# Kernel tuning notes

Hardware: AMD Instinct MI355X
Metric: run time of the kernel (lower is better)

The kernel has to match this reference:

```python
import jax, jax.numpy as jnp
import numpy as np

N, DIM = 4096, 1024

def setup_inputs() -> dict:
    key = jax.random.key(0)
    ks = jax.random.split(key, 5)
    scale = 1.0 / np.sqrt(DIM)
    return {
        "x": jax.random.normal(ks[0], (N, DIM), dtype=jnp.float32),
        "Wq": jax.random.normal(ks[1], (DIM, DIM), dtype=jnp.float32) * scale,
        "bq": jax.random.normal(ks[2], (DIM,), dtype=jnp.float32) * 0.01,
        "Wk": jax.random.normal(ks[3], (DIM, DIM), dtype=jnp.float32) * scale,
        "bk": jax.random.normal(ks[4], (DIM,), dtype=jnp.float32) * 0.01,
    }

def reference(x, Wq, bq, Wk, bk):
    # torch nn.Linear: y = x @ W.T + b
    q = x @ Wq.T + bq            # [N, D]
    k = x @ Wk.T + bk            # [N, D]
    scores = q @ k.T             # [N, N] (no 1/sqrt(d) scaling, as in source)
    attn = jax.nn.softmax(scores, axis=-1)
    return attn @ x              # weighted pooling over raw x (no value proj)
```

## Files before the change

kernel.cpp:

```cpp
#include <hip/hip_runtime.h>
#include <hip/hip_bf16.h>
#include <hip/hip_fp16.h>
#include <stdint.h>


using half8   = __attribute__((ext_vector_type(8))) _Float16;
using float4v = __attribute__((ext_vector_type(4))) float;
using int4v   = __attribute__((ext_vector_type(4))) int;

#define QS        (6.0f / 32768.0f)
#define INV_S     (32768.0f / 6.0f)
#define INV_S256  (128.0f / 6.0f)
#define C_HH      (65536.0f * QS * QS)
#define C_X       (256.0f * QS * QS)

#define SX        (6.0f / 32768.0f)
#define SW        (0.25f / 32768.0f)
#define P_HH      (65536.0f * SX * SW)
#define P_X       (256.0f * SX * SW)

#define GLOAD_LDS16(gptr, ldsptr)                                              \
  __builtin_amdgcn_global_load_lds(                                            \
      (__attribute__((address_space(1))) void*)(uintptr_t)(gptr),              \
      (__attribute__((address_space(3))) void*)(unsigned)(uintptr_t)(ldsptr),  \
      16, 0, 0)

__global__ __launch_bounds__(256, 2) void gemm_s_stats(
    const int8_t* __restrict__ Ahi, const int8_t* __restrict__ Alo,
    const int8_t* __restrict__ Bhi, const int8_t* __restrict__ Blo,
    _Float16* __restrict__ E, float2* __restrict__ stats)
{
  __shared__ __align__(16) int8_t sAh[128 * 64];
  __shared__ __align__(16) int8_t sAl[128 * 64];
  __shared__ __align__(16) int8_t sBh[128 * 64];
  __shared__ __align__(16) int8_t sBl[128 * 64];

  const int tid  = threadIdx.x;
  const int wave = tid >> 6;
  const int lane = tid & 63;
  const int quad = lane >> 4;
  const int t16  = lane & 15;
  const int wm   = wave & 1;
  const int wn   = wave >> 1;
  const int row0 = blockIdx.y * 128;
  const int col0 = blockIdx.x * 128;

  const int seg  = lane & 3;
  const int rsub = lane >> 2;

  int4v hh[4][4], cc[4][4];
#pragma unroll
  for (int i = 0; i < 4; ++i)
#pragma unroll
    for (int j = 0; j < 4; ++j) {
      hh[i][j] = (int4v){0, 0, 0, 0};
      cc[i][j] = (int4v){0, 0, 0, 0};
    }

  for (int k0 = 0; k0 < 1024; k0 += 64) {
#pragma unroll
    for (int r = 0; r < 2; ++r) {
      const int trow = r * 64 + wave * 16;
      const size_t goffA = (size_t)(row0 + trow + rsub) * 2048 + k0 + seg * 16;
      const size_t goffB = (size_t)(col0 + trow + rsub) * 2048 + k0 + seg * 16;
      GLOAD_LDS16(Ahi + goffA, &sAh[trow * 64]);
      GLOAD_LDS16(Alo + goffA, &sAl[trow * 64]);
      GLOAD_LDS16(Bhi + goffB, &sBh[trow * 64]);
      GLOAD_LDS16(Blo + goffB, &sBl[trow * 64]);
    }
    __syncthreads();

    int4v ah[4], al[4], bh[4], bl[4];
#pragma unroll
    for (int i = 0; i < 4; ++i) {
      const int ar = (wm * 64 + i * 16 + t16) * 64 + quad * 16;
      ah[i] = *(const int4v*)&sAh[ar];
      al[i] = *(const int4v*)&sAl[ar];
    }
#pragma unroll
    for (int j = 0; j < 4; ++j) {
      const int br = (wn * 64 + j * 16 + t16) * 64 + quad * 16;
      bh[j] = *(const int4v*)&sBh[br];
      bl[j] = *(const int4v*)&sBl[br];
    }

#pragma unroll
    for (int i = 0; i < 4; ++i)
#pragma unroll
      for (int j = 0; j < 4; ++j) {
        hh[i][j] = __builtin_amdgcn_mfma_i32_16x16x64_i8(ah[i], bh[j], hh[i][j], 0, 0, 0);
        cc[i][j] = __builtin_amdgcn_mfma_i32_16x16x64_i8(ah[i], bl[j], cc[i][j], 0, 0, 0);
        cc[i][j] = __builtin_amdgcn_mfma_i32_16x16x64_i8(al[i], bh[j], cc[i][j], 0, 0, 0);
      }
    __syncthreads();
  }

  float* red = (float*)sAh;

  float vv[4][4][4];
  float rmax[4][4];
#pragma unroll
  for (int i = 0; i < 4; ++i)
#pragma unroll
    for (int r = 0; r < 4; ++r) {
      float mx = -3.0e38f;
#pragma unroll
      for (int j = 0; j < 4; ++j) {
        float v = C_HH * (float)hh[i][j][r] + C_X * (float)cc[i][j][r];
        vv[i][j][r] = v;
        mx = fmaxf(mx, v);
      }
      mx = fmaxf(mx, __shfl_xor(mx, 1));
      mx = fmaxf(mx, __shfl_xor(mx, 2));
      mx = fmaxf(mx, __shfl_xor(mx, 4));
      mx = fmaxf(mx, __shfl_xor(mx, 8));
      rmax[i][r] = mx;
    }
  if (t16 == 0) {
#pragma unroll
    for (int i = 0; i < 4; ++i)
#pragma unroll
      for (int r = 0; r < 4; ++r)
        red[wn * 128 + wm * 64 + i * 16 + quad * 4 + r] = rmax[i][r];
  }
  __syncthreads();

  float mrow[4][4];
#pragma unroll
  for (int i = 0; i < 4; ++i)
#pragma unroll
    for (int r = 0; r < 4; ++r) {
      const int row = wm * 64 + i * 16 + quad * 4 + r;
      mrow[i][r] = fmaxf(red[row], red[128 + row]);
    }

  float rsum[4][4];
#pragma unroll
  for (int i = 0; i < 4; ++i)
#pragma unroll
    for (int r = 0; r < 4; ++r) {
      float s = 0.f;
#pragma unroll
      for (int j = 0; j < 4; ++j) {
        float e = __expf(vv[i][j][r] - mrow[i][r]);
        vv[i][j][r] = e;
        s += e;
      }
      s += __shfl_xor(s, 1);
      s += __shfl_xor(s, 2);
      s += __shfl_xor(s, 4);
      s += __shfl_xor(s, 8);
      rsum[i][r] = s;
    }
  if (t16 == 0) {
#pragma unroll
    for (int i = 0; i < 4; ++i)
#pragma unroll
      for (int r = 0; r < 4; ++r)
        red[256 + wn * 128 + wm * 64 + i * 16 + quad * 4 + r] = rsum[i][r];
  }
  __syncthreads();

#pragma unroll
  for (int i = 0; i < 4; ++i) {
#pragma unroll
    for (int j = 0; j < 4; ++j) {
#pragma unroll
      for (int r = 0; r < 4; ++r) {
        const int crow = row0 + wm * 64 + i * 16 + quad * 4 + r;
        const int ccol = col0 + wn * 64 + j * 16 + t16;
        E[(size_t)crow * 4096 + ccol] = (_Float16)vv[i][j][r];
      }
    }
  }
  if (wn == 0 && t16 == 0) {
#pragma unroll
    for (int i = 0; i < 4; ++i)
#pragma unroll
      for (int r = 0; r < 4; ++r) {
        const int row = wm * 64 + i * 16 + quad * 4 + r;
        const float l = red[256 + row] + red[256 + 128 + row];
        stats[(size_t)(row0 + row) * 32 + blockIdx.x] =
            make_float2(mrow[i][r], l);
      }
  }
}

__global__ __launch_bounds__(256, 2) void gemm_proj_i8(
    const int8_t* __restrict__ Ahi, const int8_t* __restrict__ Alo,
    const int8_t* __restrict__ Bhi, const int8_t* __restrict__ Blo,
    const float* __restrict__ biasQ, const float* __restrict__ biasK,
    int8_t* __restrict__ Ch, int8_t* __restrict__ Cl)
{
  __shared__ __align__(16) int8_t sAh[128 * 64];
  __shared__ __align__(16) int8_t sAl[128 * 64];
  __shared__ __align__(16) int8_t sBh[128 * 64];
  __shared__ __align__(16) int8_t sBl[128 * 64];

  const int tid  = threadIdx.x;
  const int wave = tid >> 6;
  const int lane = tid & 63;
  const int quad = lane >> 4;
  const int t16  = lane & 15;
  const int wm   = wave & 1;
  const int wn   = wave >> 1;
  const int row0 = blockIdx.y * 128;
  const int col0 = blockIdx.x * 128;

  const int seg  = lane & 3;
  const int rsub = lane >> 2;

  int4v hh[4][4], cc[4][4];
#pragma unroll
  for (int i = 0; i < 4; ++i)
#pragma unroll
    for (int j = 0; j < 4; ++j) {
      hh[i][j] = (int4v){0, 0, 0, 0};
      cc[i][j] = (int4v){0, 0, 0, 0};
    }

  for (int k0 = 0; k0 < 1024; k0 += 64) {
#pragma unroll
    for (int r = 0; r < 2; ++r) {
      const int trow = r * 64 + wave * 16;
      const size_t goffA = (size_t)(row0 + trow + rsub) * 1024 + k0 + seg * 16;
      const size_t goffB = (size_t)(col0 + trow + rsub) * 1024 + k0 + seg * 16;
      GLOAD_LDS16(Ahi + goffA, &sAh[trow * 64]);
      GLOAD_LDS16(Alo + goffA, &sAl[trow * 64]);
      GLOAD_LDS16(Bhi + goffB, &sBh[trow * 64]);
      GLOAD_LDS16(Blo + goffB, &sBl[trow * 64]);
    }
    __syncthreads();

    int4v ah[4], al[4], bh[4], bl[4];
#pragma unroll
    for (int i = 0; i < 4; ++i) {
      const int ar = (wm * 64 + i * 16 + t16) * 64 + quad * 16;
      ah[i] = *(const int4v*)&sAh[ar];
      al[i] = *(const int4v*)&sAl[ar];
    }
#pragma unroll
    for (int j = 0; j < 4; ++j) {
      const int br = (wn * 64 + j * 16 + t16) * 64 + quad * 16;
      bh[j] = *(const int4v*)&sBh[br];
      bl[j] = *(const int4v*)&sBl[br];
    }

#pragma unroll
    for (int i = 0; i < 4; ++i)
#pragma unroll
      for (int j = 0; j < 4; ++j) {
        hh[i][j] = __builtin_amdgcn_mfma_i32_16x16x64_i8(ah[i], bh[j], hh[i][j], 0, 0, 0);
        cc[i][j] = __builtin_amdgcn_mfma_i32_16x16x64_i8(ah[i], bl[j], cc[i][j], 0, 0, 0);
        cc[i][j] = __builtin_amdgcn_mfma_i32_16x16x64_i8(al[i], bh[j], cc[i][j], 0, 0, 0);
      }
    __syncthreads();
  }

#pragma unroll
  for (int i = 0; i < 4; ++i) {
#pragma unroll
    for (int j = 0; j < 4; ++j) {
      const int ccol = col0 + wn * 64 + j * 16 + t16;
      const float* bp = (ccol < 1024) ? biasQ : (biasK - 1024);
#pragma unroll
      for (int r = 0; r < 4; ++r) {
        const int crow = row0 + wm * 64 + i * 16 + quad * 4 + r;
        float v = P_HH * (float)hh[i][j][r] + P_X * (float)cc[i][j][r] + bp[ccol];
        int hi = (int)lrintf(v * INV_S256);
        hi = hi > 127 ? 127 : (hi < -127 ? -127 : hi);
        int lo = (int)lrintf(v * INV_S - 256.0f * (float)hi);
        lo = lo > 127 ? 127 : (lo < -127 ? -127 : lo);
        Ch[(size_t)crow * 2048 + ccol] = (int8_t)hi;
        Cl[(size_t)crow * 2048 + ccol] = (int8_t)lo;
      }
    }
  }
}

__global__ __launch_bounds__(512) void gemm_av(
    const uint16_t* __restrict__ E, const uint16_t* __restrict__ B,
    const float2* __restrict__ stats, float* __restrict__ out)
{
  __shared__ __align__(16) uint16_t stage[16384];
  __shared__ float betaS[128 * 33];

  const int L      = blockIdx.x;
  const int xcd    = L & 7;
  const int rest   = L >> 3;
  const int colb   = rest & 7;
  const int bandHi = rest >> 3;
  const int band   = xcd + 8 * bandHi;
  const int row0   = band * 128;
  const int col0   = colb * 128;

  const int tid  = threadIdx.x;
  const int wave = tid >> 6;
  const int z    = wave >> 2;
  const int gw   = wave & 3;
  const int lane = tid & 63;
  const int quad = lane >> 4;
  const int t16  = lane & 15;
  const int wm   = gw & 1;
  const int wn   = gw >> 1;
  const int seg  = lane & 3;
  const int rsub = lane >> 2;

  if (tid < 128) {
    const int row = row0 + tid;
    float2 st[32];
    float m = -3.0e38f;
#pragma unroll
    for (int t = 0; t < 32; ++t) {
      st[t] = stats[(size_t)row * 32 + t];
      m = fmaxf(m, st[t].x);
    }
    float l = 0.f;
#pragma unroll
    for (int t = 0; t < 32; ++t) l += st[t].y * __expf(st[t].x - m);
    const float inv = 1.0f / l;
#pragma unroll
    for (int t = 0; t < 32; ++t)
      betaS[tid * 33 + t] = __expf(st[t].x - m) * inv;
  }
  __syncthreads();

  uint16_t* sA = &stage[z * 8192];
  uint16_t* sB = &stage[z * 8192 + 4096];

  float4v acc[4][4];
#pragma unroll
  for (int i = 0; i < 4; ++i)
#pragma unroll
    for (int j = 0; j < 4; ++j)
      acc[i][j] = (float4v){0.f, 0.f, 0.f, 0.f};

  for (int tt = 0; tt < 16; ++tt) {
    const int t = z * 16 + tt;
    _Float16 bb[4];
#pragma unroll
    for (int i = 0; i < 4; ++i)
      bb[i] = (_Float16)betaS[(wm * 64 + i * 16 + t16) * 33 + t];

#pragma unroll
    for (int kk = 0; kk < 4; ++kk) {
      const int k0 = t * 128 + kk * 32;
#pragma unroll
      for (int r = 0; r < 2; ++r) {
        const int trow = r * 64 + gw * 16;
        const size_t goffA = (size_t)(row0 + trow + rsub) * 4096 + k0 + seg * 8;
        const size_t goffB = (size_t)(col0 + trow + rsub) * 4096 + k0 + seg * 8;
        GLOAD_LDS16(E + goffA, &sA[trow * 32]);
        GLOAD_LDS16(B + goffB, &sB[trow * 32]);
      }
      __syncthreads();

      half8 af[4], bf[4];
#pragma unroll
      for (int i = 0; i < 4; ++i) {
        af[i] = *(const half8*)&sA[(wm * 64 + i * 16 + t16) * 32 + quad * 8];
        half8 bs;
#pragma unroll
        for (int c = 0; c < 8; ++c) bs[c] = bb[i];
        af[i] = af[i] * bs;
      }
#pragma unroll
      for (int j = 0; j < 4; ++j)
        bf[j] = *(const half8*)&sB[(wn * 64 + j * 16 + t16) * 32 + quad * 8];

#pragma unroll
      for (int i = 0; i < 4; ++i)
#pragma unroll
        for (int j = 0; j < 4; ++j)
          acc[i][j] = __builtin_amdgcn_mfma_f32_16x16x32_f16(af[i], bf[j], acc[i][j], 0, 0, 0);
      __syncthreads();
    }
  }

  float* xfer = (float*)stage;
#pragma unroll
  for (int h = 0; h < 2; ++h) {
    if (z == 1) {
#pragma unroll
      for (int i = 2 * h; i < 2 * h + 2; ++i)
#pragma unroll
        for (int j = 0; j < 4; ++j)
#pragma unroll
          for (int r = 0; r < 4; ++r) {
            const int e = (i - 2 * h) * 16 + j * 4 + r;
            xfer[e * 256 + gw * 64 + lane] = acc[i][j][r];
          }
    }
    __syncthreads();
    if (z == 0) {
#pragma unroll
      for (int i = 2 * h; i < 2 * h + 2; ++i)
#pragma unroll
        for (int j = 0; j < 4; ++j)
#pragma unroll
          for (int r = 0; r < 4; ++r) {
            const int e = (i - 2 * h) * 16 + j * 4 + r;
            acc[i][j][r] += xfer[e * 256 + gw * 64 + lane];
          }
    }
    __syncthreads();
  }

  if (z == 0) {
#pragma unroll
    for (int i = 0; i < 4; ++i) {
#pragma unroll
      for (int j = 0; j < 4; ++j) {
        const int ccol = col0 + wn * 64 + j * 16 + t16;
#pragma unroll
        for (int r = 0; r < 4; ++r) {
          const int crow = row0 + wm * 64 + i * 16 + quad * 4 + r;
          out[(size_t)crow * 1024 + ccol] = acc[i][j][r];
        }
      }
    }
  }
}

__global__ __launch_bounds__(256) void quantT(
    const float* __restrict__ x, const float* __restrict__ Wq,
    const float* __restrict__ Wk,
    int8_t* __restrict__ xhi, int8_t* __restrict__ xlo,
    int8_t* __restrict__ whi, int8_t* __restrict__ wlo,
    uint16_t* __restrict__ xT)
{
  if (blockIdx.x < 6144) {
    int i = blockIdx.x * 256 + threadIdx.x;
    const float* src; int8_t* dh; int8_t* dl; int idx; float s256, s;
    if (i < 1048576)      { src = x;  idx = i;           dh = xhi; dl = xlo;
                            s256 = INV_S256; s = INV_S; }
    else if (i < 1310720) { src = Wq; idx = i - 1048576; dh = whi; dl = wlo;
                            s256 = 512.0f; s = 131072.0f; }
    else                  { src = Wk; idx = i - 1310720; dh = whi + 1048576;
                            dl = wlo + 1048576; s256 = 512.0f; s = 131072.0f; }
    float4 v = ((const float4*)src)[idx];
    float vv[4] = {v.x, v.y, v.z, v.w};
    int hp = 0, lp = 0;
#pragma unroll
    for (int c = 0; c < 4; ++c) {
      int h = (int)lrintf(vv[c] * s256);
      h = h > 127 ? 127 : (h < -127 ? -127 : h);
      int l = (int)lrintf(vv[c] * s - 256.0f * (float)h);
      l = l > 127 ? 127 : (l < -127 ? -127 : l);
      hp |= (h & 0xff) << (8 * c);
      lp |= (l & 0xff) << (8 * c);
    }
    ((int*)dh)[idx] = hp;
    ((int*)dl)[idx] = lp;
  } else {
    __shared__ float tile[32][33];
    const int tb = blockIdx.x - 6144;
    const int bx = tb & 31;
    const int by = tb >> 5;
    const int tx = threadIdx.x & 31;
    const int ty = threadIdx.x >> 5;
#pragma unroll
    for (int p = 0; p < 4; ++p) {
      const int row = by * 32 + ty + p * 8;
      tile[ty + p * 8][tx] = x[(size_t)row * 1024 + bx * 32 + tx];
    }
    __syncthreads();
#pragma unroll
    for (int p = 0; p < 4; ++p) {
      const int oc = ty + p * 8;
      __half hv = __float2half_rn(tile[tx][oc]);
      xT[(size_t)(bx * 32 + oc) * 4096 + by * 32 + tx] = *(uint16_t*)&hv;
    }
  }
}

extern "C" void kernel_launch(void* const* d_in, const int* in_sizes, int n_in,
                              void* d_out, int out_size, void* d_ws, size_t ws_size,
                              hipStream_t stream) {
  const int N = 4096, D = 1024;
  const float* x  = (const float*)d_in[0];
  const float* Wq = (const float*)d_in[1];
  const float* bq = (const float*)d_in[2];
  const float* Wk = (const float*)d_in[3];
  const float* bk = (const float*)d_in[4];
  float* out = (float*)d_out;

  char* w = (char*)d_ws;
  const size_t MiB = 1024 * 1024;
  int8_t*    xq_hi  = (int8_t*)   (w + 0  * MiB);
  int8_t*    xq_lo  = (int8_t*)   (w + 4  * MiB);
  int8_t*    Wqk_hi = (int8_t*)   (w + 8  * MiB);
  int8_t*    Wqk_lo = (int8_t*)   (w + 10 * MiB);
  int8_t*    qk_hi  = (int8_t*)   (w + 12 * MiB);
  int8_t*    qk_lo  = (int8_t*)   (w + 20 * MiB);
  _Float16*  E      = (_Float16*) (w + 36 * MiB);
  float2*    stats  = (float2*)   (w + 68 * MiB);
  uint16_t*  xTh    = (uint16_t*) (w + 72 * MiB);

  quantT<<<10240, 256, 0, stream>>>(x, Wq, Wk, xq_hi, xq_lo, Wqk_hi, Wqk_lo,
                                    xTh);

  gemm_proj_i8<<<dim3(2048 / 128, N / 128), 256, 0, stream>>>(
      xq_hi, xq_lo, Wqk_hi, Wqk_lo, bq, bk, qk_hi, qk_lo);

  gemm_s_stats<<<dim3(N / 128, N / 128), 256, 0, stream>>>(
      qk_hi, qk_lo, qk_hi + 1024, qk_lo + 1024, E, stats);

  gemm_av<<<256, 512, 0, stream>>>((const uint16_t*)E, xTh, stats, out);

  (void)in_sizes; (void)n_in; (void)out_size; (void)ws_size;
}
```

Measured before the change: 242.5 us.

## Split gemm_av K across four blocks with atomic accumulation

Replaces the intra-block two-group split-K with LDS reduction by a 4-way split-K across separate blocks, quadrupling the grid to 1024 blocks of 256 threads. Partial results are accumulated into the output with float atomicAdd, and the output is zeroed with a memset beforehand. This aims to raise occupancy and parallelism for the attention-times-x GEMM. It adds atomic traffic, a memset pass, redundant per-block softmax stat reduction, and nondeterministic summation order.

```diff
diff --git a/kernel.cpp b/kernel.cpp
--- a/kernel.cpp
+++ b/kernel.cpp
@@ -278,31 +278,31 @@
   }
 }
 
-__global__ __launch_bounds__(512) void gemm_av(
+__global__ __launch_bounds__(256) void gemm_av(
     const uint16_t* __restrict__ E, const uint16_t* __restrict__ B,
     const float2* __restrict__ stats, float* __restrict__ out)
 {
-  __shared__ __align__(16) uint16_t stage[16384];
+  __shared__ __align__(16) uint16_t sA[128 * 32];
+  __shared__ __align__(16) uint16_t sB[128 * 32];
   __shared__ float betaS[128 * 33];
 
   const int L      = blockIdx.x;
   const int xcd    = L & 7;
-  const int rest   = L >> 3;
-  const int colb   = rest & 7;
-  const int bandHi = rest >> 3;
+  const int inner  = (L >> 3) & 31;
+  const int bandHi = L >> 8;
   const int band   = xcd + 8 * bandHi;
+  const int colb   = inner & 7;
+  const int z      = inner >> 3;
   const int row0   = band * 128;
   const int col0   = colb * 128;
 
   const int tid  = threadIdx.x;
   const int wave = tid >> 6;
-  const int z    = wave >> 2;
-  const int gw   = wave & 3;
   const int lane = tid & 63;
   const int quad = lane >> 4;
   const int t16  = lane & 15;
-  const int wm   = gw & 1;
-  const int wn   = gw >> 1;
+  const int wm   = wave & 1;
+  const int wn   = wave >> 1;
   const int seg  = lane & 3;
   const int rsub = lane >> 2;
 
@@ -325,9 +325,6 @@
   }
   __syncthreads();
 
-  uint16_t* sA = &stage[z * 8192];
-  uint16_t* sB = &stage[z * 8192 + 4096];
-
   float4v acc[4][4];
 #pragma unroll
   for (int i = 0; i < 4; ++i)
@@ -335,8 +332,8 @@
     for (int j = 0; j < 4; ++j)
       acc[i][j] = (float4v){0.f, 0.f, 0.f, 0.f};
 
-  for (int tt = 0; tt < 16; ++tt) {
-    const int t = z * 16 + tt;
+  for (int tt = 0; tt < 8; ++tt) {
+    const int t = z * 8 + tt;
     _Float16 bb[4];
 #pragma unroll
     for (int i = 0; i < 4; ++i)
@@ -347,7 +344,7 @@
       const int k0 = t * 128 + kk * 32;
 #pragma unroll
       for (int r = 0; r < 2; ++r) {
-        const int trow = r * 64 + gw * 16;
+        const int trow = r * 64 + wave * 16;
         const size_t goffA = (size_t)(row0 + trow + rsub) * 4096 + k0 + seg * 8;
         const size_t goffB = (size_t)(col0 + trow + rsub) * 4096 + k0 + seg * 8;
         GLOAD_LDS16(E + goffA, &sA[trow * 32]);
@@ -377,46 +374,15 @@
     }
   }
 
-  float* xfer = (float*)stage;
-#pragma unroll
-  for (int h = 0; h < 2; ++h) {
-    if (z == 1) {
-#pragma unroll
-      for (int i = 2 * h; i < 2 * h + 2; ++i)
-#pragma unroll
-        for (int j = 0; j < 4; ++j)
-#pragma unroll
-          for (int r = 0; r < 4; ++r) {
-            const int e = (i - 2 * h) * 16 + j * 4 + r;
-            xfer[e * 256 + gw * 64 + lane] = acc[i][j][r];
-          }
-    }
-    __syncthreads();
-    if (z == 0) {
-#pragma unroll
-      for (int i = 2 * h; i < 2 * h + 2; ++i)
-#pragma unroll
-        for (int j = 0; j < 4; ++j)
-#pragma unroll
-          for (int r = 0; r < 4; ++r) {
-            const int e = (i - 2 * h) * 16 + j * 4 + r;
-            acc[i][j][r] += xfer[e * 256 + gw * 64 + lane];
-          }
-    }
-    __syncthreads();
-  }
-
-  if (z == 0) {
-#pragma unroll
-    for (int i = 0; i < 4; ++i) {
-#pragma unroll
-      for (int j = 0; j < 4; ++j) {
-        const int ccol = col0 + wn * 64 + j * 16 + t16;
-#pragma unroll
-        for (int r = 0; r < 4; ++r) {
-          const int crow = row0 + wm * 64 + i * 16 + quad * 4 + r;
-          out[(size_t)crow * 1024 + ccol] = acc[i][j][r];
-        }
+#pragma unroll
+  for (int i = 0; i < 4; ++i) {
+#pragma unroll
+    for (int j = 0; j < 4; ++j) {
+      const int ccol = col0 + wn * 64 + j * 16 + t16;
+#pragma unroll
+      for (int r = 0; r < 4; ++r) {
+        const int crow = row0 + wm * 64 + i * 16 + quad * 4 + r;
+        atomicAdd(&out[(size_t)crow * 1024 + ccol], acc[i][j][r]);
       }
     }
   }
@@ -497,6 +463,8 @@
   float2*    stats  = (float2*)   (w + 68 * MiB);
   uint16_t*  xTh    = (uint16_t*) (w + 72 * MiB);
 
+  hipMemsetAsync(out, 0, (size_t)N * D * sizeof(float), stream);
+
   quantT<<<10240, 256, 0, stream>>>(x, Wq, Wk, xq_hi, xq_lo, Wqk_hi, Wqk_lo,
                                     xTh);
 
@@ -506,7 +474,7 @@
   gemm_s_stats<<<dim3(N / 128, N / 128), 256, 0, stream>>>(
       qk_hi, qk_lo, qk_hi + 1024, qk_lo + 1024, E, stats);
 
-  gemm_av<<<256, 512, 0, stream>>>((const uint16_t*)E, xTh, stats, out);
+  gemm_av<<<1024, 256, 0, stream>>>((const uint16_t*)E, xTh, stats, out);
 
   (void)in_sizes; (void)n_in; (void)out_size; (void)ws_size;
 }
```

Measured after the change: 275.6 us. +13.6%, slower.

## Retile attn@x GEMM to 128x64 tiles with 512 blocks of 256 threads

Applied to the files above, without the earlier changes.

Splits the final attention-times-x GEMM into 128x64 output tiles, doubling the grid to 512 blocks of 4 waves each (two K-groups of two waves) instead of 256 blocks of 8 waves. It also stores the softmax rescale factors in LDS as fp16 and restructures the staging loads so each wave issues a share of the A/B tile copies per 32-wide K step. The aim is better occupancy and CU coverage on the 256-CU part. The cost is that each E row band is reloaded by twice as many blocks, so more global/L2 traffic for A.

```diff
diff --git a/kernel.cpp b/kernel.cpp
--- a/kernel.cpp
+++ b/kernel.cpp
@@ -278,31 +278,29 @@
   }
 }
 
-__global__ __launch_bounds__(512) void gemm_av(
+__global__ __launch_bounds__(256) void gemm_av(
     const uint16_t* __restrict__ E, const uint16_t* __restrict__ B,
     const float2* __restrict__ stats, float* __restrict__ out)
 {
-  __shared__ __align__(16) uint16_t stage[16384];
-  __shared__ float betaS[128 * 33];
+  __shared__ __align__(16) uint16_t stage[12288];
+  __shared__ _Float16 betaS[128 * 33];
 
   const int L      = blockIdx.x;
   const int xcd    = L & 7;
   const int rest   = L >> 3;
-  const int colb   = rest & 7;
-  const int bandHi = rest >> 3;
+  const int colb   = rest & 15;
+  const int bandHi = rest >> 4;
   const int band   = xcd + 8 * bandHi;
   const int row0   = band * 128;
-  const int col0   = colb * 128;
+  const int col0   = colb * 64;
 
   const int tid  = threadIdx.x;
   const int wave = tid >> 6;
-  const int z    = wave >> 2;
-  const int gw   = wave & 3;
+  const int kg   = wave >> 1;
+  const int wm   = wave & 1;
   const int lane = tid & 63;
   const int quad = lane >> 4;
   const int t16  = lane & 15;
-  const int wm   = gw & 1;
-  const int wn   = gw >> 1;
   const int seg  = lane & 3;
   const int rsub = lane >> 2;
 
@@ -321,12 +319,12 @@
     const float inv = 1.0f / l;
 #pragma unroll
     for (int t = 0; t < 32; ++t)
-      betaS[tid * 33 + t] = __expf(st[t].x - m) * inv;
+      betaS[tid * 33 + t] = (_Float16)(__expf(st[t].x - m) * inv);
   }
   __syncthreads();
 
-  uint16_t* sA = &stage[z * 8192];
-  uint16_t* sB = &stage[z * 8192 + 4096];
+  uint16_t* sAg = &stage[kg * 4096];
+  uint16_t* sBg = &stage[8192 + kg * 2048];
 
   float4v acc[4][4];
 #pragma unroll
@@ -335,83 +333,89 @@
     for (int j = 0; j < 4; ++j)
       acc[i][j] = (float4v){0.f, 0.f, 0.f, 0.f};
 
-  for (int tt = 0; tt < 16; ++tt) {
-    const int t = z * 16 + tt;
-    _Float16 bb[4];
+  _Float16 bb[4];
+
+  for (int it = 0; it < 64; ++it) {
+    if ((it & 3) == 0) {
+      const int t = kg * 16 + (it >> 2);
+#pragma unroll
+      for (int i = 0; i < 4; ++i)
+        bb[i] = betaS[(wm * 64 + i * 16 + t16) * 33 + t];
+    }
+
+#pragma unroll
+    for (int r = 0; r < 6; ++r) {
+      const int p = wave * 6 + r;
+      if (p < 16) {
+        const int g    = p >> 3;
+        const int trow = (p & 7) * 16;
+        const int k0   = g * 2048 + it * 32;
+        const size_t goff = (size_t)(row0 + trow + rsub) * 4096 + k0 + seg * 8;
+        GLOAD_LDS16(E + goff, &stage[g * 4096 + trow * 32]);
+      } else {
+        const int q    = p - 16;
+        const int g    = q >> 2;
+        const int trow = (q & 3) * 16;
+        const int k0   = g * 2048 + it * 32;
+        const size_t goff = (size_t)(col0 + trow + rsub) * 4096 + k0 + seg * 8;
+        GLOAD_LDS16(B + goff, &stage[8192 + g * 2048 + trow * 32]);
+      }
+    }
+    __syncthreads();
+
+    half8 af[4], bf[4];
+#pragma unroll
+    for (int i = 0; i < 4; ++i) {
+      half8 bs;
+#pragma unroll
+      for (int c = 0; c < 8; ++c) bs[c] = bb[i];
+      af[i] = *(const half8*)&sAg[(wm * 64 + i * 16 + t16) * 32 + quad * 8] * bs;
+    }
+#pragma unroll
+    for (int j = 0; j < 4; ++j)
+      bf[j] = *(const half8*)&sBg[(j * 16 + t16) * 32 + quad * 8];
+
 #pragma unroll
     for (int i = 0; i < 4; ++i)
-      bb[i] = (_Float16)betaS[(wm * 64 + i * 16 + t16) * 33 + t];
-
-#pragma unroll
-    for (int kk = 0; kk < 4; ++kk) {
-      const int k0 = t * 128 + kk * 32;
-#pragma unroll
-      for (int r = 0; r < 2; ++r) {
-        const int trow = r * 64 + gw * 16;
-        const size_t goffA = (size_t)(row0 + trow + rsub) * 4096 + k0 + seg * 8;
-        const size_t goffB = (size_t)(col0 + trow + rsub) * 4096 + k0 + seg * 8;
-        GLOAD_LDS16(E + goffA, &sA[trow * 32]);
-        GLOAD_LDS16(B + goffB, &sB[trow * 32]);
-      }
-      __syncthreads();
-
-      half8 af[4], bf[4];
-#pragma unroll
-      for (int i = 0; i < 4; ++i) {
-        af[i] = *(const half8*)&sA[(wm * 64 + i * 16 + t16) * 32 + quad * 8];
-        half8 bs;
-#pragma unroll
-        for (int c = 0; c < 8; ++c) bs[c] = bb[i];
-        af[i] = af[i] * bs;
-      }
 #pragma unroll
       for (int j = 0; j < 4; ++j)
-        bf[j] = *(const half8*)&sB[(wn * 64 + j * 16 + t16) * 32 + quad * 8];
-
-#pragma unroll
-      for (int i = 0; i < 4; ++i)
+        acc[i][j] = __builtin_amdgcn_mfma_f32_16x16x32_f16(af[i], bf[j], acc[i][j], 0, 0, 0);
+    __syncthreads();
+  }
+
+  float* xfer = (float*)stage;
+#pragma unroll
+  for (int h = 0; h < 2; ++h) {
+    if (kg == 1) {
+#pragma unroll
+      for (int ii = 0; ii < 2; ++ii)
 #pragma unroll
         for (int j = 0; j < 4; ++j)
-          acc[i][j] = __builtin_amdgcn_mfma_f32_16x16x32_f16(af[i], bf[j], acc[i][j], 0, 0, 0);
-      __syncthreads();
-    }
-  }
-
-  float* xfer = (float*)stage;
-#pragma unroll
-  for (int h = 0; h < 2; ++h) {
-    if (z == 1) {
-#pragma unroll
-      for (int i = 2 * h; i < 2 * h + 2; ++i)
+#pragma unroll
+          for (int r = 0; r < 4; ++r)
+            xfer[wm * 2048 + ((ii * 4 + j) * 4 + r) * 64 + lane] =
+                acc[2 * h + ii][j][r];
+    }
+    __syncthreads();
+    if (kg == 0) {
+#pragma unroll
+      for (int ii = 0; ii < 2; ++ii)
 #pragma unroll
         for (int j = 0; j < 4; ++j)
 #pragma unroll
-          for (int r = 0; r < 4; ++r) {
-            const int e = (i - 2 * h) * 16 + j * 4 + r;
-            xfer[e * 256 + gw * 64 + lane] = acc[i][j][r];
-          }
-    }
-    __syncthreads();
-    if (z == 0) {
-#pragma unroll
-      for (int i = 2 * h; i < 2 * h + 2; ++i)
-#pragma unroll
-        for (int j = 0; j < 4; ++j)
-#pragma unroll
-          for (int r = 0; r < 4; ++r) {
-            const int e = (i - 2 * h) * 16 + j * 4 + r;
-            acc[i][j][r] += xfer[e * 256 + gw * 64 + lane];
-          }
-    }
-    __syncthreads();
-  }
-
-  if (z == 0) {
+          for (int r = 0; r < 4; ++r)
+            acc[2 * h + ii][j][r] +=
+                xfer[wm * 2048 + ((ii * 4 + j) * 4 + r) * 64 + lane];
+    }
+    __syncthreads();
+  }
+
+  if (kg == 0) {
 #pragma unroll
     for (int i = 0; i < 4; ++i) {
 #pragma unroll
       for (int j = 0; j < 4; ++j) {
-        const int ccol = col0 + wn * 64 + j * 16 + t16;
+        const int ccol = col0 + j * 16 + t16;
 #pragma unroll
         for (int r = 0; r < 4; ++r) {
           const int crow = row0 + wm * 64 + i * 16 + quad * 4 + r;
@@ -506,7 +510,7 @@
   gemm_s_stats<<<dim3(N / 128, N / 128), 256, 0, stream>>>(
       qk_hi, qk_lo, qk_hi + 1024, qk_lo + 1024, E, stats);
 
-  gemm_av<<<256, 512, 0, stream>>>((const uint16_t*)E, xTh, stats, out);
+  gemm_av<<<512, 256, 0, stream>>>((const uint16_t*)E, xTh, stats, out);
 
   (void)in_sizes; (void)n_in; (void)out_size; (void)ws_size;
 }
```

Result: no change. 242.8 us (+0.1%).
